# Performance work log

Hardware: AMD Instinct MI355X
Metric: run time of the kernel (lower is better)

## Reference

```python
import math
import jax, jax.numpy as jnp
import numpy as np

B, L, D, H, INNER = 8, 1024, 256, 8, 1024
HD = D // H
EPS = 1e-12


def _ln(x, g, b):
    m = jnp.mean(x, axis=-1, keepdims=True)
    v = jnp.mean((x - m) ** 2, axis=-1, keepdims=True)
    return (x - m) / jnp.sqrt(v + EPS) * g + b


def setup_inputs() -> dict:
    key = jax.random.key(0)
    ks = jax.random.split(key, 16)
    def lin(k, out_d, in_d):
        s = 1.0 / math.sqrt(in_d)
        kw, kb = jax.random.split(k)
        return (jax.random.uniform(kw, (out_d, in_d), jnp.float32, -s, s),
                jax.random.uniform(kb, (out_d,), jnp.float32, -s, s))
    Wq, bq = lin(ks[0], D, D)
    Wk, bk = lin(ks[1], D, D)
    Wv, bv = lin(ks[2], D, D)
    Wo, bo = lin(ks[3], D, D)
    W1, b1 = lin(ks[4], INNER, D)
    W2, b2 = lin(ks[5], D, INNER)
    return {
        'hidden_states': jax.random.normal(ks[6], (B, L, D), jnp.float32),
        'attention_mask': jnp.zeros((B, 1, 1, L), jnp.float32),
        'phi': jax.random.uniform(ks[7], (B, H, L), jnp.float32, 0.0, 2.0 * math.pi),
        'mag': jax.random.uniform(ks[8], (B, H, L), jnp.float32),
        'Wq': Wq, 'bq': bq, 'Wk': Wk, 'bk': bk, 'Wv': Wv, 'bv': bv,
        'Wo': Wo, 'bo': bo,
        'ln1_g': jnp.ones((D,), jnp.float32), 'ln1_b': jnp.zeros((D,), jnp.float32),
        'gamma': jnp.full((1, H, 1, 1), 0.1, jnp.float32),
        'W1': W1, 'b1': b1, 'W2': W2, 'b2': b2,
        'ln2_g': jnp.ones((D,), jnp.float32), 'ln2_b': jnp.zeros((D,), jnp.float32),
    }


def reference(hidden_states, attention_mask, phi, mag, Wq, bq, Wk, bk, Wv, bv,
              Wo, bo, ln1_g, ln1_b, gamma, W1, b1, W2, b2, ln2_g, ln2_b):
    residual = hidden_states
    def shape(x):  # [B,L,D] -> [B,H,L,hd]
        return x.reshape(B, L, H, HD).transpose(0, 2, 1, 3)
    q = shape(hidden_states @ Wq.T + bq)
    k = shape(hidden_states @ Wk.T + bk)
    v = shape(hidden_states @ Wv.T + bv)
    semantic = jnp.einsum('bhld,bhmd->bhlm', q, k) / math.sqrt(HD)
    # physics: gamma * (mag_i*mag_j) * cos(phi_i - phi_j), per band/head
    physics = gamma * (mag[..., :, None] * mag[..., None, :]) * jnp.cos(phi[..., :, None] - phi[..., None, :])
    scores = semantic + physics + attention_mask
    eye = jnp.eye(L, dtype=bool)[None, None]
    row_max = jnp.max(scores, axis=-1, keepdims=True)
    scores = jnp.where(row_max <= -1e8, jnp.where(eye, 0.0, scores), scores)
    probs = jax.nn.softmax(scores, axis=-1)
    ctx = jnp.einsum('bhlm,bhmd->bhld', probs, v).transpose(0, 2, 1, 3).reshape(B, L, D)
    attn_out = _ln(ctx @ Wo.T + bo + residual, ln1_g, ln1_b)
    h = attn_out @ W1.T + b1
    h = h * 0.5 * (1.0 + jax.lax.erf(h / math.sqrt(2.0)))  # exact-erf gelu as in source
    return _ln(h @ W2.T + b2 + attn_out, ln2_g, ln2_b)
```

## Files before the change

### kernel.cpp

```cpp
#include <hip/hip_runtime.h>
#include <hip/hip_bf16.h>
#include <math.h>

typedef __attribute__((ext_vector_type(8))) short bf16x8;
typedef __attribute__((ext_vector_type(4))) float f32x4;
typedef __attribute__((ext_vector_type(16))) float f32x16;

__device__ __forceinline__ unsigned short f2bf(float f) {
  union { float f; unsigned u; } v; v.f = f;
  unsigned r = v.u + 0x7fffu + ((v.u >> 16) & 1u);
  return (unsigned short)(r >> 16);
}
__device__ __forceinline__ unsigned pack2(float lo, float hi) {
  return (unsigned)f2bf(lo) | ((unsigned)f2bf(hi) << 16);
}
__device__ __forceinline__ float bf2f(unsigned short u) {
  union { unsigned u; float f; } v; v.u = ((unsigned)u) << 16; return v.f;
}
__device__ __forceinline__ float fexp2(float x) {
#if __has_builtin(__builtin_amdgcn_exp2f)
  return __builtin_amdgcn_exp2f(x);
#else
  return exp2f(x);
#endif
}
__device__ __forceinline__ unsigned cvtpk(float lo, float hi) {
  unsigned r;
  asm("v_cvt_pk_bf16_f32 %0, %1, %2" : "=v"(r) : "v"(lo), "v"(hi));
  return r;
}
__device__ __forceinline__ void gload16(const void* gsrc, void* lds) {
  __builtin_amdgcn_global_load_lds(
      (const __attribute__((address_space(1))) unsigned int*)gsrc,
      (__attribute__((address_space(3))) unsigned int*)lds, 16, 0, 0);
}
#if __has_builtin(__builtin_amdgcn_permlane32_swap)
typedef __attribute__((ext_vector_type(2))) unsigned u32x2;
__device__ __forceinline__ void plswap(unsigned& a, unsigned& b) {
  u32x2 r = __builtin_amdgcn_permlane32_swap(a, b, false, false);
  a = r[0]; b = r[1];
}
#else
__device__ __forceinline__ void plswap(unsigned& a, unsigned& b) {
  unsigned as = (unsigned)__shfl_xor((int)a, 32, 64);
  unsigned bs = (unsigned)__shfl_xor((int)b, 32, 64);
  bool hi = (threadIdx.x & 32) != 0;
  unsigned na = hi ? bs : a;
  unsigned nb = hi ? b : as;
  a = na; b = nb;
}
#endif

#define L2E 1.4426950408889634f

__device__ __forceinline__ int xcd_swz(int p, int cpx) {
  return (p & 7) * cpx + (p >> 3);
}

__global__ __launch_bounds__(256) void prep_kernel(
    const float* __restrict__ hs, const float* __restrict__ phi,
    const float* __restrict__ mag, const float* __restrict__ mask,
    const float* __restrict__ gamma, const float* __restrict__ Wq,
    const float* __restrict__ Wk, const float* __restrict__ Wv,
    const float* __restrict__ Wo, const float* __restrict__ W1,
    const float* __restrict__ W2, unsigned short* __restrict__ wts,
    unsigned short* __restrict__ hsb, unsigned short* __restrict__ qx,
    unsigned short* __restrict__ kx) {
  const int blk = blockIdx.x, tid = threadIdx.x;
  if (blk < 768) {
    int i = blk * 1024 + tid * 4;
    const float* src; int off;
    if (i < 262144) {
      src = (i < 131072) ? (i < 65536 ? Wq : Wk) : (i < 196608 ? Wv : Wo);
      off = i & 65535;
    } else if (i < 524288) { src = W1; off = i - 262144; }
    else { src = W2; off = i - 524288; }
    float4 v = *(const float4*)&src[off];
    *(uint2*)&wts[i] = make_uint2(pack2(v.x, v.y), pack2(v.z, v.w));
  } else if (blk < 1792) {
    int i = (blk - 768) * 2048 + tid * 8;
    const float4* hp = (const float4*)hs;
    float4 a = hp[i >> 2], b = hp[(i >> 2) + 1];
    uint4 o = make_uint4(pack2(a.x, a.y), pack2(a.z, a.w), pack2(b.x, b.y),
                         pack2(b.z, b.w));
    *(uint4*)&hsb[i] = o;
  } else {
    int row = (blk - 1792) * 256 + tid;
    int bh = row >> 10, key = row & 1023, b = row >> 13, h = (row >> 10) & 7;
    float p = phi[row], mg = mag[row];
    float sn, cs; sincosf(p, &sn, &cs);
    float c = mg * cs, s = mg * sn;
    float msk = mask[b * 1024 + key];
    int ch = key >> 5, k32 = key & 31;
    size_t base = ((((size_t)(bh * 32 + ch) * 3 + 2) * 2 + 0) * 32 + k32) * 8;
    *(uint4*)&kx[base] = make_uint4(pack2(c, s), pack2(msk, 0.0f), 0u, 0u);
    *(uint4*)&kx[base + 256] = make_uint4(0u, 0u, 0u, 0u);
    float g = gamma[h];
    *(uint4*)&qx[base] = make_uint4(pack2(L2E * g * c, L2E * g * s),
                                    pack2(L2E, 0.0f), 0u, 0u);
    *(uint4*)&qx[base + 256] = make_uint4(0u, 0u, 0u, 0u);
  }
}

__global__ __launch_bounds__(256) void gemm_qkv(
    const unsigned short* __restrict__ A, const unsigned short* __restrict__ wts,
    const float* __restrict__ bq, const float* __restrict__ bk,
    const float* __restrict__ bv, unsigned short* __restrict__ qx,
    unsigned short* __restrict__ kx, unsigned short* __restrict__ vt2) {
  __shared__ __align__(16) unsigned short As[128 * 64];
  __shared__ __align__(16) unsigned short Bs[128 * 64];
  const int tid = threadIdx.x;
  const int w_id = xcd_swz(blockIdx.x, 48);
  const int xw = w_id % 6;
  const int mat = xw >> 1;
  const int n0 = (xw & 1) * 128;
  const int m0 = (w_id / 6) * 128;
  const unsigned short* W = wts + mat * 65536;
  const float* bias = (mat == 0) ? bq : ((mat == 1) ? bk : bv);
  const int wm = (tid >> 7) & 1, wn = (tid >> 6) & 1;
  const int g = (tid >> 4) & 3, c = tid & 15;
  const int l = tid & 63, wv = tid >> 6;
  const int rr = l >> 3, scol = ((l & 7) ^ rr) << 3;
  const unsigned short* aSrc = &A[(size_t)(m0 + wv * 32 + rr) * 256 + scol];
  const unsigned short* bSrc = &W[(size_t)(n0 + wv * 32 + rr) * 256 + scol];
  unsigned short* aDst = &As[wv * 32 * 64];
  unsigned short* bDst = &Bs[wv * 32 * 64];
  f32x4 acc[4][4] = {};
  for (int k0 = 0; k0 < 256; k0 += 64) {
    __syncthreads();
#pragma unroll
    for (int i = 0; i < 4; i++) {
      gload16(aSrc + (size_t)i * 8 * 256 + k0, aDst + i * 8 * 64);
      gload16(bSrc + (size_t)i * 8 * 256 + k0, bDst + i * 8 * 64);
    }
    __syncthreads();
#pragma unroll
    for (int kk = 0; kk < 2; kk++) {
      bf16x8 af[4], bfr[4];
#pragma unroll
      for (int mi = 0; mi < 4; mi++) {
        int row = wm * 64 + mi * 16 + c;
        af[mi] = *(const bf16x8*)&As[row * 64 + (((g + 4 * kk) ^ (row & 7)) << 3)];
      }
#pragma unroll
      for (int ni = 0; ni < 4; ni++) {
        int row = wn * 64 + ni * 16 + c;
        bfr[ni] = *(const bf16x8*)&Bs[row * 64 + (((g + 4 * kk) ^ (row & 7)) << 3)];
      }
#pragma unroll
      for (int mi = 0; mi < 4; mi++)
#pragma unroll
        for (int ni = 0; ni < 4; ni++)
          acc[mi][ni] = __builtin_amdgcn_mfma_f32_16x16x32_bf16(af[mi], bfr[ni], acc[mi][ni], 0, 0, 0);
    }
  }
  const float scale = (mat == 0) ? (L2E * 0.17677669529663687f) : 1.0f;
#pragma unroll
  for (int ni = 0; ni < 4; ni++) {
    int n = n0 + wn * 64 + ni * 16 + c;
    float bv_ = bias[n];
    int h = n >> 5, dd = n & 31;
#pragma unroll
    for (int mi = 0; mi < 4; mi++) {
      int mbase = m0 + wm * 64 + mi * 16 + 4 * g;
      int bb = mbase >> 10, rowL = mbase & 1023;
      int bh = bb * 8 + h;
      if (mat < 2) {
        unsigned short* out = (mat == 0) ? qx : kx;
        int m_idx = dd >> 4, hi = (dd >> 3) & 1, j = dd & 7;
#pragma unroll
        for (int r = 0; r < 4; r++) {
          int keyL = rowL + r;
          int ch = keyL >> 5, k32 = keyL & 31;
          out[(((((size_t)bh * 32 + ch) * 3 + m_idx) * 2 + hi) * 32 + k32) * 8 + j] =
              f2bf((acc[mi][ni][r] + bv_) * scale);
        }
      } else {
        int keyL = rowL;
        int ch = keyL >> 5, t = (keyL >> 4) & 1, hi = (keyL >> 3) & 1;
        size_t base = (((((size_t)bh * 32 + ch) * 2 + t) * 2 + hi) * 32 + dd) * 8 + (g & 1) * 4;
        uint2 w2 = make_uint2(pack2(acc[mi][ni][0] + bv_, acc[mi][ni][1] + bv_),
                              pack2(acc[mi][ni][2] + bv_, acc[mi][ni][3] + bv_));
        *(uint2*)&vt2[base] = w2;
      }
    }
  }
}

__global__ __launch_bounds__(256) void attn32(
    const unsigned short* __restrict__ qx, const unsigned short* __restrict__ kx,
    const unsigned short* __restrict__ vt2, unsigned short* __restrict__ ctx) {
  const int tid = threadIdx.x;
  const int wave = tid >> 6, lane = tid & 63;
  const int hi = lane >> 5, l31 = lane & 31;
  const int w_id = xcd_swz(blockIdx.x, 64);
  const int bh = w_id >> 3, bb = bh >> 3, h = bh & 7;
  const int qch = (w_id & 7) * 4 + wave;

  const size_t qoff = (((size_t)(bh * 32 + qch) * 3 * 2 + hi) * 32 + l31) * 8;
  bf16x8 qf0 = *(const bf16x8*)&qx[qoff];
  bf16x8 qf1 = *(const bf16x8*)&qx[qoff + 512];
  bf16x8 qf2 = *(const bf16x8*)&qx[qoff + 1024];

  f32x16 acc = {};
  float mrun = 0.0f, lsum = 0.0f;

  for (int ch = 0; ch < 32; ch++) {
    const size_t koff = (((size_t)(bh * 32 + ch) * 3 * 2 + hi) * 32 + l31) * 8;
    bf16x8 kf0 = *(const bf16x8*)&kx[koff];
    bf16x8 kf1 = *(const bf16x8*)&kx[koff + 512];
    bf16x8 kf2 = *(const bf16x8*)&kx[koff + 1024];
    const size_t voff = (((size_t)(bh * 32 + ch) * 2 * 2 + hi) * 32 + l31) * 8;
    bf16x8 vf0 = *(const bf16x8*)&vt2[voff];
    bf16x8 vf1 = *(const bf16x8*)&vt2[voff + 512];

    f32x16 s = {};
    __builtin_amdgcn_s_setprio(1);
    s = __builtin_amdgcn_mfma_f32_32x32x16_bf16(kf0, qf0, s, 0, 0, 0);
    s = __builtin_amdgcn_mfma_f32_32x32x16_bf16(kf1, qf1, s, 0, 0, 0);
    s = __builtin_amdgcn_mfma_f32_32x32x16_bf16(kf2, qf2, s, 0, 0, 0);
    __builtin_amdgcn_s_setprio(0);

    float pm = fmaxf(fmaxf(fmaxf(s[0], s[1]), fmaxf(s[2], s[3])),
                     fmaxf(fmaxf(s[4], s[5]), fmaxf(s[6], s[7])));
    pm = fmaxf(pm, fmaxf(fmaxf(fmaxf(s[8], s[9]), fmaxf(s[10], s[11])),
                         fmaxf(fmaxf(s[12], s[13]), fmaxf(s[14], s[15]))));
    pm = fmaxf(pm, __shfl_xor(pm, 32, 64));
    if (__any(pm > mrun + 12.0f)) {
      float mn = fmaxf(mrun, pm);
      float rs = fexp2(mrun - mn);
      lsum *= rs;
      mrun = mn;
#pragma unroll
      for (int r = 0; r < 16; r++) {
        float rr = __shfl(rs, (r & 3) + 8 * (r >> 2) + 4 * hi, 64);
        acc[r] *= rr;
      }
    }
    float p[16];
#pragma unroll
    for (int r = 0; r < 16; r++) p[r] = fexp2(s[r] - mrun);
    lsum += (((p[0] + p[1]) + (p[2] + p[3])) + ((p[4] + p[5]) + (p[6] + p[7]))) +
            (((p[8] + p[9]) + (p[10] + p[11])) + ((p[12] + p[13]) + (p[14] + p[15])));
    unsigned u0 = cvtpk(p[0], p[1]), u1 = cvtpk(p[2], p[3]);
    unsigned u2 = cvtpk(p[4], p[5]), u3 = cvtpk(p[6], p[7]);
    plswap(u0, u2); plswap(u1, u3);
    unsigned u4 = cvtpk(p[8], p[9]), u5 = cvtpk(p[10], p[11]);
    unsigned u6 = cvtpk(p[12], p[13]), u7 = cvtpk(p[14], p[15]);
    plswap(u4, u6); plswap(u5, u7);
    union { unsigned u[4]; bf16x8 v; } A1, A2;
    A1.u[0] = u0; A1.u[1] = u1; A1.u[2] = u2; A1.u[3] = u3;
    A2.u[0] = u4; A2.u[1] = u5; A2.u[2] = u6; A2.u[3] = u7;
    __builtin_amdgcn_s_setprio(1);
    acc = __builtin_amdgcn_mfma_f32_32x32x16_bf16(A1.v, vf0, acc, 0, 0, 0);
    acc = __builtin_amdgcn_mfma_f32_32x32x16_bf16(A2.v, vf1, acc, 0, 0, 0);
    __builtin_amdgcn_s_setprio(0);
  }
  lsum += __shfl_xor(lsum, 32, 64);
  float inv = 1.0f / lsum;
#pragma unroll
  for (int r = 0; r < 16; r++) {
    int qr = (r & 3) + 8 * (r >> 2) + 4 * hi;
    float rr = __shfl(inv, qr, 64);
    ctx[((size_t)bb * 1024 + qch * 32 + qr) * 256 + h * 32 + l31] = f2bf(acc[r] * rr);
  }
}

template <int KD, int RESBF, int OUTBF>
__global__ __launch_bounds__(512) void gemm_ln(
    const unsigned short* __restrict__ A, const unsigned short* __restrict__ W,
    const float* __restrict__ bias, const void* __restrict__ resid,
    const float* __restrict__ lng, const float* __restrict__ lnb,
    void* __restrict__ out) {
  __shared__ __align__(16) unsigned short As[16 * 64];
  __shared__ __align__(16) unsigned short Bs[256 * 64];
  __shared__ float red[2][8][16];
  const int tid = threadIdx.x;
  const int w_id = xcd_swz(blockIdx.x, 64);
  const int m0 = w_id * 16;
  const int w = tid >> 6, l = tid & 63;
  const int g = (l >> 4) & 3, c = l & 15;
  const int rr = l >> 3, scol = ((l & 7) ^ rr) << 3;
  const unsigned short* aSrc = &A[(size_t)(m0 + rr) * KD + scol];
  const unsigned short* bSrc = &W[(size_t)(w * 32 + rr) * KD + scol];
  unsigned short* bDst = &Bs[w * 32 * 64];
  f32x4 acc[2] = {};
  for (int k0 = 0; k0 < KD; k0 += 64) {
    __syncthreads();
    if (w == 0) {
      gload16(aSrc + k0, &As[0]);
      gload16(aSrc + (size_t)8 * KD + k0, &As[8 * 64]);
    }
#pragma unroll
    for (int i = 0; i < 4; i++)
      gload16(bSrc + (size_t)i * 8 * KD + k0, bDst + i * 8 * 64);
    __syncthreads();
#pragma unroll
    for (int kk = 0; kk < 2; kk++) {
      bf16x8 af = *(const bf16x8*)&As[c * 64 + (((g + 4 * kk) ^ (c & 7)) << 3)];
#pragma unroll
      for (int ni = 0; ni < 2; ni++) {
        int row = w * 32 + ni * 16 + c;
        bf16x8 bfr = *(const bf16x8*)&Bs[row * 64 + (((g + 4 * kk) ^ (row & 7)) << 3)];
        acc[ni] = __builtin_amdgcn_mfma_f32_16x16x32_bf16(af, bfr, acc[ni], 0, 0, 0);
      }
    }
  }
  float x[2][4], s1[4], s2[4];
#pragma unroll
  for (int r = 0; r < 4; r++) { s1[r] = 0.0f; s2[r] = 0.0f; }
#pragma unroll
  for (int ni = 0; ni < 2; ni++) {
    int n = w * 32 + ni * 16 + c;
    float bv_ = bias[n];
#pragma unroll
    for (int r = 0; r < 4; r++) {
      int m = m0 + 4 * g + r;
      float rv = RESBF
          ? bf2f(((const unsigned short*)resid)[(size_t)m * 256 + n])
          : ((const float*)resid)[(size_t)m * 256 + n];
      float v = acc[ni][r] + bv_ + rv;
      x[ni][r] = v;
      s1[r] += v;
      s2[r] += v * v;
    }
  }
#pragma unroll
  for (int off = 1; off < 16; off <<= 1) {
#pragma unroll
    for (int r = 0; r < 4; r++) {
      s1[r] += __shfl_xor(s1[r], off, 64);
      s2[r] += __shfl_xor(s2[r], off, 64);
    }
  }
  if (c == 0) {
#pragma unroll
    for (int r = 0; r < 4; r++) {
      red[0][w][4 * g + r] = s1[r];
      red[1][w][4 * g + r] = s2[r];
    }
  }
  __syncthreads();
#pragma unroll
  for (int r = 0; r < 4; r++) {
    int row = 4 * g + r;
    float t1 = 0.0f, t2 = 0.0f;
#pragma unroll
    for (int ww = 0; ww < 8; ww++) { t1 += red[0][ww][row]; t2 += red[1][ww][row]; }
    float mean = t1 * (1.0f / 256.0f);
    float var = fmaxf(t2 * (1.0f / 256.0f) - mean * mean, 0.0f);
    float istd = rsqrtf(var + 1e-12f);
    int m = m0 + row;
#pragma unroll
    for (int ni = 0; ni < 2; ni++) {
      int n = w * 32 + ni * 16 + c;
      float o = (x[ni][r] - mean) * istd * lng[n] + lnb[n];
      if constexpr (OUTBF)
        ((unsigned short*)out)[(size_t)m * 256 + n] = f2bf(o);
      else
        ((float*)out)[(size_t)m * 256 + n] = o;
    }
  }
}

__global__ __launch_bounds__(256) void gemm_ffn1(
    const unsigned short* __restrict__ A, const unsigned short* __restrict__ W,
    const float* __restrict__ bias, unsigned short* __restrict__ Cout,
    int N, int K) {
  __shared__ __align__(16) unsigned short As[128 * 64];
  __shared__ __align__(16) unsigned short Bs[128 * 64];
  const int tid = threadIdx.x;
  const int w_id = xcd_swz(blockIdx.x, 64);
  const int n0 = (w_id % 8) * 128;
  const int m0 = (w_id / 8) * 128;
  const int wm = (tid >> 7) & 1, wn = (tid >> 6) & 1;
  const int g = (tid >> 4) & 3, c = tid & 15;
  const int l = tid & 63, wv = tid >> 6;
  const int rr = l >> 3, scol = ((l & 7) ^ rr) << 3;
  const unsigned short* aSrc = &A[(size_t)(m0 + wv * 32 + rr) * K + scol];
  const unsigned short* bSrc = &W[(size_t)(n0 + wv * 32 + rr) * K + scol];
  unsigned short* aDst = &As[wv * 32 * 64];
  unsigned short* bDst = &Bs[wv * 32 * 64];
  f32x4 acc[4][4] = {};
  for (int k0 = 0; k0 < K; k0 += 64) {
    __syncthreads();
#pragma unroll
    for (int i = 0; i < 4; i++) {
      gload16(aSrc + (size_t)i * 8 * K + k0, aDst + i * 8 * 64);
      gload16(bSrc + (size_t)i * 8 * K + k0, bDst + i * 8 * 64);
    }
    __syncthreads();
#pragma unroll
    for (int kk = 0; kk < 2; kk++) {
      bf16x8 af[4], bfr[4];
#pragma unroll
      for (int mi = 0; mi < 4; mi++) {
        int row = wm * 64 + mi * 16 + c;
        af[mi] = *(const bf16x8*)&As[row * 64 + (((g + 4 * kk) ^ (row & 7)) << 3)];
      }
#pragma unroll
      for (int ni = 0; ni < 4; ni++) {
        int row = wn * 64 + ni * 16 + c;
        bfr[ni] = *(const bf16x8*)&Bs[row * 64 + (((g + 4 * kk) ^ (row & 7)) << 3)];
      }
#pragma unroll
      for (int mi = 0; mi < 4; mi++)
#pragma unroll
        for (int ni = 0; ni < 4; ni++)
          acc[mi][ni] = __builtin_amdgcn_mfma_f32_16x16x32_bf16(af[mi], bfr[ni], acc[mi][ni], 0, 0, 0);
    }
  }
#pragma unroll
  for (int ni = 0; ni < 4; ni++) {
    int n = n0 + wn * 64 + ni * 16 + c;
    float bv_ = bias[n];
#pragma unroll
    for (int mi = 0; mi < 4; mi++) {
      int mbase = m0 + wm * 64 + mi * 16 + 4 * g;
#pragma unroll
      for (int r = 0; r < 4; r++) {
        int m = mbase + r;
        float x = acc[mi][ni][r] + bv_;
        Cout[(size_t)m * N + n] =
            f2bf(x * 0.5f * (1.0f + erff(x * 0.70710678118654752f)));
      }
    }
  }
}

extern "C" void kernel_launch(void* const* d_in, const int* in_sizes, int n_in,
                              void* d_out, int out_size, void* d_ws,
                              size_t ws_size, hipStream_t stream) {
  const float* hs = (const float*)d_in[0];
  const float* mask = (const float*)d_in[1];
  const float* phi = (const float*)d_in[2];
  const float* mag = (const float*)d_in[3];
  const float* Wq = (const float*)d_in[4];
  const float* bq = (const float*)d_in[5];
  const float* Wk = (const float*)d_in[6];
  const float* bk = (const float*)d_in[7];
  const float* Wv = (const float*)d_in[8];
  const float* bv = (const float*)d_in[9];
  const float* Wo = (const float*)d_in[10];
  const float* bo = (const float*)d_in[11];
  const float* ln1g = (const float*)d_in[12];
  const float* ln1b = (const float*)d_in[13];
  const float* gamma = (const float*)d_in[14];
  const float* W1 = (const float*)d_in[15];
  const float* b1 = (const float*)d_in[16];
  const float* W2 = (const float*)d_in[17];
  const float* b2 = (const float*)d_in[18];
  const float* ln2g = (const float*)d_in[19];
  const float* ln2b = (const float*)d_in[20];

  char* wsb = (char*)d_ws;
  unsigned short* wts = (unsigned short*)(wsb + 0);
  unsigned short* hsb = (unsigned short*)(wsb + (2ull << 20));
  unsigned short* ctx = (unsigned short*)(wsb + (6ull << 20));
  unsigned short* aout = (unsigned short*)(wsb + (10ull << 20));
  unsigned short* qx = (unsigned short*)(wsb + (22ull << 20));
  unsigned short* kx = (unsigned short*)(wsb + (28ull << 20));
  unsigned short* vt2 = (unsigned short*)(wsb + (34ull << 20));
  unsigned short* hbuf = (unsigned short*)(wsb + (22ull << 20));

  dim3 blk(256);
  prep_kernel<<<dim3(2048), blk, 0, stream>>>(hs, phi, mag, mask, gamma, Wq, Wk,
                                              Wv, Wo, W1, W2, wts, hsb, qx, kx);
  gemm_qkv<<<dim3(384), blk, 0, stream>>>(hsb, wts, bq, bk, bv, qx, kx, vt2);
  attn32<<<dim3(512), blk, 0, stream>>>(qx, kx, vt2, ctx);
  gemm_ln<256, 0, 1><<<dim3(512), dim3(512), 0, stream>>>(
      ctx, wts + 196608, bo, hs, ln1g, ln1b, aout);
  gemm_ffn1<<<dim3(512), blk, 0, stream>>>(aout, wts + 262144, b1, hbuf, 1024, 256);
  gemm_ln<1024, 1, 0><<<dim3(512), dim3(512), 0, stream>>>(
      hbuf, wts + 524288, b2, aout, ln2g, ln2b, d_out);
}
```

Before: 94.87 us.

## Eliminate prep kernel by fusing conversions into QKV GEMM and attention launches

Removes the standalone prep kernel. The QKV GEMM now reads fp32 hidden states and weights directly and converts them to bf16 while staging into LDS, and it computes the phi/mag physics columns in 64 extra blocks. The Wo/W1/W2 bf16 conversion moves into 576 extra blocks appended to the attention launch, so it overlaps with attention. This saves a launch and a bf16 hidden-state round trip, at the cost of register-staged loads in place of async global-to-LDS loads and twice the fp32 global traffic in the GEMM. hbuf is moved to its own workspace region.

```diff
diff --git a/kernel.cpp b/kernel.cpp
--- a/kernel.cpp
+++ b/kernel.cpp
@@ -5,6 +5,8 @@
 typedef __attribute__((ext_vector_type(8))) short bf16x8;
 typedef __attribute__((ext_vector_type(4))) float f32x4;
 typedef __attribute__((ext_vector_type(16))) float f32x16;
+
+#define L2E 1.4426950408889634f
 
 __device__ __forceinline__ unsigned short f2bf(float f) {
   union { float f; unsigned u; } v; v.f = f;
@@ -28,6 +30,10 @@
   unsigned r;
   asm("v_cvt_pk_bf16_f32 %0, %1, %2" : "=v"(r) : "v"(lo), "v"(hi));
   return r;
+}
+__device__ __forceinline__ uint4 pack8(float4 a, float4 b) {
+  return make_uint4(pack2(a.x, a.y), pack2(a.z, a.w), pack2(b.x, b.y),
+                    pack2(b.z, b.w));
 }
 __device__ __forceinline__ void gload16(const void* gsrc, void* lds) {
   __builtin_amdgcn_global_load_lds(
@@ -51,87 +57,66 @@
 }
 #endif
 
-#define L2E 1.4426950408889634f
-
 __device__ __forceinline__ int xcd_swz(int p, int cpx) {
   return (p & 7) * cpx + (p >> 3);
 }
 
-__global__ __launch_bounds__(256) void prep_kernel(
-    const float* __restrict__ hs, const float* __restrict__ phi,
+__global__ __launch_bounds__(256) void gemm_qkv(
+    const float* __restrict__ A, const float* __restrict__ Wq,
+    const float* __restrict__ Wk, const float* __restrict__ Wv,
+    const float* __restrict__ bq, const float* __restrict__ bk,
+    const float* __restrict__ bv, const float* __restrict__ phi,
     const float* __restrict__ mag, const float* __restrict__ mask,
-    const float* __restrict__ gamma, const float* __restrict__ Wq,
-    const float* __restrict__ Wk, const float* __restrict__ Wv,
-    const float* __restrict__ Wo, const float* __restrict__ W1,
-    const float* __restrict__ W2, unsigned short* __restrict__ wts,
-    unsigned short* __restrict__ hsb, unsigned short* __restrict__ qx,
-    unsigned short* __restrict__ kx) {
-  const int blk = blockIdx.x, tid = threadIdx.x;
-  if (blk < 768) {
-    int i = blk * 1024 + tid * 4;
-    const float* src; int off;
-    if (i < 262144) {
-      src = (i < 131072) ? (i < 65536 ? Wq : Wk) : (i < 196608 ? Wv : Wo);
-      off = i & 65535;
-    } else if (i < 524288) { src = W1; off = i - 262144; }
-    else { src = W2; off = i - 524288; }
-    float4 v = *(const float4*)&src[off];
-    *(uint2*)&wts[i] = make_uint2(pack2(v.x, v.y), pack2(v.z, v.w));
-  } else if (blk < 1792) {
-    int i = (blk - 768) * 2048 + tid * 8;
-    const float4* hp = (const float4*)hs;
-    float4 a = hp[i >> 2], b = hp[(i >> 2) + 1];
-    uint4 o = make_uint4(pack2(a.x, a.y), pack2(a.z, a.w), pack2(b.x, b.y),
-                         pack2(b.z, b.w));
-    *(uint4*)&hsb[i] = o;
-  } else {
-    int row = (blk - 1792) * 256 + tid;
-    int bh = row >> 10, key = row & 1023, b = row >> 13, h = (row >> 10) & 7;
-    float p = phi[row], mg = mag[row];
-    float sn, cs; sincosf(p, &sn, &cs);
-    float c = mg * cs, s = mg * sn;
-    float msk = mask[b * 1024 + key];
-    int ch = key >> 5, k32 = key & 31;
-    size_t base = ((((size_t)(bh * 32 + ch) * 3 + 2) * 2 + 0) * 32 + k32) * 8;
-    *(uint4*)&kx[base] = make_uint4(pack2(c, s), pack2(msk, 0.0f), 0u, 0u);
-    *(uint4*)&kx[base + 256] = make_uint4(0u, 0u, 0u, 0u);
-    float g = gamma[h];
-    *(uint4*)&qx[base] = make_uint4(pack2(L2E * g * c, L2E * g * s),
-                                    pack2(L2E, 0.0f), 0u, 0u);
-    *(uint4*)&qx[base + 256] = make_uint4(0u, 0u, 0u, 0u);
-  }
-}
-
-__global__ __launch_bounds__(256) void gemm_qkv(
-    const unsigned short* __restrict__ A, const unsigned short* __restrict__ wts,
-    const float* __restrict__ bq, const float* __restrict__ bk,
-    const float* __restrict__ bv, unsigned short* __restrict__ qx,
+    const float* __restrict__ gamma, unsigned short* __restrict__ qx,
     unsigned short* __restrict__ kx, unsigned short* __restrict__ vt2) {
+  const int tid = threadIdx.x;
+  const int p = blockIdx.x;
+  if (p >= 384) {
+    const int bh = p - 384, b = bh >> 3, h = bh & 7;
+    const float gm = gamma[h];
+#pragma unroll
+    for (int rr = 0; rr < 4; rr++) {
+      int key = tid * 4 + rr;
+      int row = bh * 1024 + key;
+      float pp = phi[row], mg = mag[row];
+      float sn, cs; sincosf(pp, &sn, &cs);
+      float c = mg * cs, s = mg * sn;
+      float msk = mask[b * 1024 + key];
+      int ch = key >> 5, k32 = key & 31;
+      size_t base = ((((size_t)(bh * 32 + ch) * 3 + 2) * 2 + 0) * 32 + k32) * 8;
+      *(uint4*)&kx[base] = make_uint4(pack2(c, s), pack2(msk, 0.0f), 0u, 0u);
+      *(uint4*)&kx[base + 256] = make_uint4(0u, 0u, 0u, 0u);
+      *(uint4*)&qx[base] = make_uint4(pack2(L2E * gm * c, L2E * gm * s),
+                                      pack2(L2E, 0.0f), 0u, 0u);
+      *(uint4*)&qx[base + 256] = make_uint4(0u, 0u, 0u, 0u);
+    }
+    return;
+  }
   __shared__ __align__(16) unsigned short As[128 * 64];
   __shared__ __align__(16) unsigned short Bs[128 * 64];
-  const int tid = threadIdx.x;
-  const int w_id = xcd_swz(blockIdx.x, 48);
+  const int w_id = xcd_swz(p, 48);
   const int xw = w_id % 6;
   const int mat = xw >> 1;
   const int n0 = (xw & 1) * 128;
   const int m0 = (w_id / 6) * 128;
-  const unsigned short* W = wts + mat * 65536;
+  const float* W = (mat == 0) ? Wq : ((mat == 1) ? Wk : Wv);
   const float* bias = (mat == 0) ? bq : ((mat == 1) ? bk : bv);
   const int wm = (tid >> 7) & 1, wn = (tid >> 6) & 1;
   const int g = (tid >> 4) & 3, c = tid & 15;
-  const int l = tid & 63, wv = tid >> 6;
-  const int rr = l >> 3, scol = ((l & 7) ^ rr) << 3;
-  const unsigned short* aSrc = &A[(size_t)(m0 + wv * 32 + rr) * 256 + scol];
-  const unsigned short* bSrc = &W[(size_t)(n0 + wv * 32 + rr) * 256 + scol];
-  unsigned short* aDst = &As[wv * 32 * 64];
-  unsigned short* bDst = &Bs[wv * 32 * 64];
   f32x4 acc[4][4] = {};
   for (int k0 = 0; k0 < 256; k0 += 64) {
     __syncthreads();
 #pragma unroll
     for (int i = 0; i < 4; i++) {
-      gload16(aSrc + (size_t)i * 8 * 256 + k0, aDst + i * 8 * 64);
-      gload16(bSrc + (size_t)i * 8 * 256 + k0, bDst + i * 8 * 64);
+      int idx = tid * 8 + i * 2048;
+      int r = idx >> 6, c8 = idx & 63;
+      const float* ap = &A[(size_t)(m0 + r) * 256 + k0 + c8];
+      const float* wp = &W[(size_t)(n0 + r) * 256 + k0 + c8];
+      float4 a0 = *(const float4*)ap, a1 = *(const float4*)(ap + 4);
+      float4 w0 = *(const float4*)wp, w1 = *(const float4*)(wp + 4);
+      int dst = r * 64 + (((c8 >> 3) ^ (r & 7)) << 3);
+      *(uint4*)&As[dst] = pack8(a0, a1);
+      *(uint4*)&Bs[dst] = pack8(w0, w1);
     }
     __syncthreads();
 #pragma unroll
@@ -179,9 +164,9 @@
         int keyL = rowL;
         int ch = keyL >> 5, t = (keyL >> 4) & 1, hi = (keyL >> 3) & 1;
         size_t base = (((((size_t)bh * 32 + ch) * 2 + t) * 2 + hi) * 32 + dd) * 8 + (g & 1) * 4;
-        uint2 w2 = make_uint2(pack2(acc[mi][ni][0] + bv_, acc[mi][ni][1] + bv_),
-                              pack2(acc[mi][ni][2] + bv_, acc[mi][ni][3] + bv_));
-        *(uint2*)&vt2[base] = w2;
+        *(uint2*)&vt2[base] =
+            make_uint2(pack2(acc[mi][ni][0] + bv_, acc[mi][ni][1] + bv_),
+                       pack2(acc[mi][ni][2] + bv_, acc[mi][ni][3] + bv_));
       }
     }
   }
@@ -189,11 +174,24 @@
 
 __global__ __launch_bounds__(256) void attn32(
     const unsigned short* __restrict__ qx, const unsigned short* __restrict__ kx,
-    const unsigned short* __restrict__ vt2, unsigned short* __restrict__ ctx) {
+    const unsigned short* __restrict__ vt2, unsigned short* __restrict__ ctx,
+    const float* __restrict__ Wo, const float* __restrict__ W1,
+    const float* __restrict__ W2, unsigned short* __restrict__ wts) {
   const int tid = threadIdx.x;
+  const int p = blockIdx.x;
+  if (p >= 512) {
+    int i = (p - 512) * 1024 + tid * 4;
+    const float* src; int off;
+    if (i < 65536) { src = Wo; off = i; }
+    else if (i < 327680) { src = W1; off = i - 65536; }
+    else { src = W2; off = i - 327680; }
+    float4 v = *(const float4*)&src[off];
+    *(uint2*)&wts[i] = make_uint2(pack2(v.x, v.y), pack2(v.z, v.w));
+    return;
+  }
   const int wave = tid >> 6, lane = tid & 63;
   const int hi = lane >> 5, l31 = lane & 31;
-  const int w_id = xcd_swz(blockIdx.x, 64);
+  const int w_id = xcd_swz(p, 64);
   const int bh = w_id >> 3, bb = bh >> 3, h = bh & 7;
   const int qch = (w_id & 7) * 4 + wave;
 
@@ -237,16 +235,16 @@
         acc[r] *= rr;
       }
     }
-    float p[16];
-#pragma unroll
-    for (int r = 0; r < 16; r++) p[r] = fexp2(s[r] - mrun);
-    lsum += (((p[0] + p[1]) + (p[2] + p[3])) + ((p[4] + p[5]) + (p[6] + p[7]))) +
-            (((p[8] + p[9]) + (p[10] + p[11])) + ((p[12] + p[13]) + (p[14] + p[15])));
-    unsigned u0 = cvtpk(p[0], p[1]), u1 = cvtpk(p[2], p[3]);
-    unsigned u2 = cvtpk(p[4], p[5]), u3 = cvtpk(p[6], p[7]);
+    float pv[16];
+#pragma unroll
+    for (int r = 0; r < 16; r++) pv[r] = fexp2(s[r] - mrun);
+    lsum += (((pv[0] + pv[1]) + (pv[2] + pv[3])) + ((pv[4] + pv[5]) + (pv[6] + pv[7]))) +
+            (((pv[8] + pv[9]) + (pv[10] + pv[11])) + ((pv[12] + pv[13]) + (pv[14] + pv[15])));
+    unsigned u0 = cvtpk(pv[0], pv[1]), u1 = cvtpk(pv[2], pv[3]);
+    unsigned u2 = cvtpk(pv[4], pv[5]), u3 = cvtpk(pv[6], pv[7]);
     plswap(u0, u2); plswap(u1, u3);
-    unsigned u4 = cvtpk(p[8], p[9]), u5 = cvtpk(p[10], p[11]);
-    unsigned u6 = cvtpk(p[12], p[13]), u7 = cvtpk(p[14], p[15]);
+    unsigned u4 = cvtpk(pv[8], pv[9]), u5 = cvtpk(pv[10], pv[11]);
+    unsigned u6 = cvtpk(pv[12], pv[13]), u7 = cvtpk(pv[14], pv[15]);
     plswap(u4, u6); plswap(u5, u7);
     union { unsigned u[4]; bf16x8 v; } A1, A2;
     A1.u[0] = u0; A1.u[1] = u1; A1.u[2] = u2; A1.u[3] = u3;
@@ -455,22 +453,20 @@
 
   char* wsb = (char*)d_ws;
   unsigned short* wts = (unsigned short*)(wsb + 0);
-  unsigned short* hsb = (unsigned short*)(wsb + (2ull << 20));
   unsigned short* ctx = (unsigned short*)(wsb + (6ull << 20));
   unsigned short* aout = (unsigned short*)(wsb + (10ull << 20));
   unsigned short* qx = (unsigned short*)(wsb + (22ull << 20));
   unsigned short* kx = (unsigned short*)(wsb + (28ull << 20));
   unsigned short* vt2 = (unsigned short*)(wsb + (34ull << 20));
-  unsigned short* hbuf = (unsigned short*)(wsb + (22ull << 20));
+  unsigned short* hbuf = (unsigned short*)(wsb + (40ull << 20));
 
   dim3 blk(256);
-  prep_kernel<<<dim3(2048), blk, 0, stream>>>(hs, phi, mag, mask, gamma, Wq, Wk,
-                                              Wv, Wo, W1, W2, wts, hsb, qx, kx);
-  gemm_qkv<<<dim3(384), blk, 0, stream>>>(hsb, wts, bq, bk, bv, qx, kx, vt2);
-  attn32<<<dim3(512), blk, 0, stream>>>(qx, kx, vt2, ctx);
+  gemm_qkv<<<dim3(448), blk, 0, stream>>>(hs, Wq, Wk, Wv, bq, bk, bv, phi,
+                                          mag, mask, gamma, qx, kx, vt2);
+  attn32<<<dim3(1088), blk, 0, stream>>>(qx, kx, vt2, ctx, Wo, W1, W2, wts);
   gemm_ln<256, 0, 1><<<dim3(512), dim3(512), 0, stream>>>(
-      ctx, wts + 196608, bo, hs, ln1g, ln1b, aout);
-  gemm_ffn1<<<dim3(512), blk, 0, stream>>>(aout, wts + 262144, b1, hbuf, 1024, 256);
+      ctx, wts, bo, hs, ln1g, ln1b, aout);
+  gemm_ffn1<<<dim3(512), blk, 0, stream>>>(aout, wts + 65536, b1, hbuf, 1024, 256);
   gemm_ln<1024, 1, 0><<<dim3(512), dim3(512), 0, stream>>>(
-      hbuf, wts + 524288, b2, aout, ln2g, ln2b, d_out);
-}
+      hbuf, wts + 327680, b2, aout, ln2g, ln2b, d_out);
+}
```

Result: faster. 90.79 us, median of 2 (-4.3%).
